# Optimization experiments

Hardware: AMD Instinct MI355X
Metric: run time of the kernel (lower is better)

Reference implementation:

```python
import jax, jax.numpy as jnp
import numpy as np

NUM_HEADS = 4
BN_EPS = 1e-5


def setup_inputs() -> dict:
    key = jax.random.key(0)
    k1, k2, k3 = jax.random.split(key, 3)
    B, C, H, W = 4, 512, 64, 64
    c_attn = 256
    x = jax.random.normal(k1, (B, C, H, W), dtype=jnp.float32)
    # 1x1 convs are plain channel matmuls: weight[out, in]
    w_qkv = jax.random.normal(k2, (3 * c_attn, c_attn), dtype=jnp.float32) * (c_attn ** -0.5)
    w_proj = jax.random.normal(k3, (c_attn, c_attn), dtype=jnp.float32) * (c_attn ** -0.5)
    gamma = jnp.ones((c_attn,), dtype=jnp.float32)
    beta = jnp.zeros((c_attn,), dtype=jnp.float32)
    return {"x": x, "w_qkv": w_qkv, "w_proj": w_proj, "gamma": gamma, "beta": beta}


def reference(x, w_qkv, w_proj, gamma, beta):
    B, C, H, W = x.shape
    c_attn = w_proj.shape[0]
    head_dim = c_attn // NUM_HEADS
    scale = head_dim ** -0.5
    N = H * W

    x_attn = x[:, :c_attn].reshape(B, c_attn, N)   # [B, c_attn, N]
    x_skip = x[:, c_attn:]                          # [B, c_skip, H, W]

    # 1x1 conv qkv (no bias): [B, 3*c_attn, N]
    qkv = jnp.einsum('oc,bcn->bon', w_qkv, x_attn)
    qkv = qkv.reshape(B, 3, NUM_HEADS, head_dim, N)
    q, k, v = qkv[:, 0], qkv[:, 1], qkv[:, 2]       # each [B, h, d, N]

    # attn[b,h,i,j] = sum_d q[b,h,d,i] * k[b,h,d,j] * scale
    attn = jnp.einsum('bhdn,bhdm->bhnm', q, k) * scale
    attn = jax.nn.softmax(attn, axis=-1)

    # out[b,h,d,i] = sum_j attn[b,h,i,j] * v[b,h,d,j]
    out = jnp.einsum('bhnm,bhdm->bhdn', attn, v).reshape(B, c_attn, N)

    # 1x1 conv proj (no bias)
    out = jnp.einsum('oc,bcn->bon', w_proj, out)

    # BatchNorm2d (training mode: batch statistics over B and spatial dims)
    mean = out.mean(axis=(0, 2), keepdims=True)
    var = out.var(axis=(0, 2), keepdims=True)  # biased variance, as torch BN
    out = (out - mean) * jax.lax.rsqrt(var + BN_EPS)
    out = out * gamma[None, :, None] + beta[None, :, None]

    out = out.reshape(B, c_attn, H, W)
    return jnp.concatenate([out, x_skip], axis=1)
```

## Files before the change

kernel.cpp:

```cpp
#include <hip/hip_runtime.h>
#include <stdint.h>

typedef float          f32x4  __attribute__((ext_vector_type(4)));
typedef __bf16         bf16x8 __attribute__((ext_vector_type(8)));
typedef unsigned short u16x4  __attribute__((ext_vector_type(4)));
typedef unsigned short u16x8  __attribute__((ext_vector_type(8)));

__device__ __forceinline__ float bf2f(unsigned short u) {
    union { uint32_t i; float f; } v; v.i = ((uint32_t)u) << 16; return v.f;
}
__device__ __forceinline__ unsigned short bfc(float f) {
    return __builtin_bit_cast(unsigned short, (__bf16)f);
}
__device__ __forceinline__ f32x4 mfma16(bf16x8 a, bf16x8 b, f32x4 c) {
    return __builtin_amdgcn_mfma_f32_16x16x32_bf16(a, b, c, 0, 0, 0);
}
__device__ __forceinline__ void async16(const unsigned short* g, unsigned short* l) {
    __builtin_amdgcn_global_load_lds(
        (const __attribute__((address_space(1))) void*)g,
        (__attribute__((address_space(3))) void*)l, 16, 0, 0);
}

#define QSC 0.18033688f

__global__ __launch_bounds__(256) void qkv_gemm(
    const float* __restrict__ x, const float* __restrict__ wqkv,
    unsigned short* __restrict__ Qb, unsigned short* __restrict__ Kb,
    unsigned short* __restrict__ Vb) {
    const int mt = blockIdx.x;
    const int nt = blockIdx.y;
    const int b  = blockIdx.z;
    const int o0 = mt * 128, n0 = nt * 128;
    __shared__ __align__(16) unsigned short Wt[128 * 72];
    __shared__ __align__(16) unsigned short Xt[128 * 72];
    const int t = threadIdx.x;
    const int lane = t & 63, w = t >> 6;
    const int wr = w >> 1, wc = w & 1;
    const int l15 = lane & 15, g = lane >> 4;

    f32x4 acc[4][4];
    const f32x4 zero = {0.f, 0.f, 0.f, 0.f};
    for (int i = 0; i < 4; i++) for (int j = 0; j < 4; j++) acc[i][j] = zero;

    for (int k0 = 0; k0 < 256; k0 += 64) {
        {
            const int row = t >> 3, col = (t & 7) * 8;
            #pragma unroll
            for (int r = 0; r < 4; r++) {
                const float* p = wqkv + (size_t)(o0 + row + r * 32) * 256 + k0 + col;
                f32x4 v0 = *(const f32x4*)p;
                f32x4 v1 = *(const f32x4*)(p + 4);
                u16x8 o8 = { bfc(v0[0]), bfc(v0[1]), bfc(v0[2]), bfc(v0[3]),
                             bfc(v1[0]), bfc(v1[1]), bfc(v1[2]), bfc(v1[3]) };
                *(u16x8*)(&Wt[(row + r * 32) * 72 + col]) = o8;
            }
        }
        {
            const int cl = t >> 4, nl = (t & 15) * 8;
            #pragma unroll
            for (int r = 0; r < 4; r++) {
                const int c = k0 + cl + r * 16;
                const float* p = x + (size_t)(b * 512 + c) * 4096 + n0 + nl;
                f32x4 v0 = *(const f32x4*)p;
                f32x4 v1 = *(const f32x4*)(p + 4);
                #pragma unroll
                for (int j = 0; j < 4; j++) Xt[(nl + j) * 72 + cl + r * 16] = bfc(v0[j]);
                #pragma unroll
                for (int j = 0; j < 4; j++) Xt[(nl + 4 + j) * 72 + cl + r * 16] = bfc(v1[j]);
            }
        }
        __syncthreads();
        #pragma unroll
        for (int kk = 0; kk < 2; kk++) {
            bf16x8 af[4], bfr[4];
            #pragma unroll
            for (int i = 0; i < 4; i++)
                af[i] = *(const bf16x8*)(&Wt[(wr * 64 + i * 16 + l15) * 72 + kk * 32 + g * 8]);
            #pragma unroll
            for (int j = 0; j < 4; j++)
                bfr[j] = *(const bf16x8*)(&Xt[(wc * 64 + j * 16 + l15) * 72 + kk * 32 + g * 8]);
            #pragma unroll
            for (int i = 0; i < 4; i++)
                #pragma unroll
                for (int j = 0; j < 4; j++)
                    acc[i][j] = mfma16(af[i], bfr[j], acc[i][j]);
        }
        __syncthreads();
    }

    #pragma unroll
    for (int i = 0; i < 4; i++) {
        const int o = o0 + wr * 64 + i * 16 + g * 4;
        #pragma unroll
        for (int j = 0; j < 4; j++) {
            const int n = n0 + wc * 64 + j * 16 + l15;
            f32x4 a = acc[i][j];
            if (o < 256) {
                u16x4 pv = { bfc(a[0] * QSC), bfc(a[1] * QSC), bfc(a[2] * QSC), bfc(a[3] * QSC) };
                const int h = o >> 6, d = o & 63;
                *(u16x4*)(&Qb[(((size_t)(b * 4 + h)) * 4096 + n) * 64 + d]) = pv;
            } else if (o < 512) {
                u16x4 pv = { bfc(a[0]), bfc(a[1]), bfc(a[2]), bfc(a[3]) };
                const int oo = o - 256; const int h = oo >> 6, d = oo & 63;
                *(u16x4*)(&Kb[(((size_t)(b * 4 + h)) * 4096 + n) * 64 + d]) = pv;
            } else {
                const int oo = o - 512; const int h = oo >> 6, d = oo & 63;
                const size_t base = (((size_t)(b * 4 + h)) * 64 + d) * 4096 + n;
                Vb[base] = bfc(a[0]); Vb[base + 4096] = bfc(a[1]);
                Vb[base + 8192] = bfc(a[2]); Vb[base + 12288] = bfc(a[3]);
            }
        }
    }
}

__global__ __launch_bounds__(256, 2) void flash_attn(
    const unsigned short* __restrict__ Qb, const unsigned short* __restrict__ Kb,
    const unsigned short* __restrict__ Vb, unsigned short* __restrict__ Opart,
    float* __restrict__ ml) {
    __shared__ __align__(16) unsigned short Kt[2][64 * 64];
    __shared__ __align__(16) unsigned short Vt[2][64 * 64];

    const int flat = (blockIdx.z * 16 + blockIdx.y) * 16 + blockIdx.x;
    const int nf = (flat & 7) * 64 + (flat >> 3);
    const int z  = nf >> 8;
    const int bh = (nf >> 4) & 15;
    const int nb = nf & 15;

    const int t = threadIdx.x, lane = t & 63, w = t >> 6;
    const int l15 = lane & 15, g = lane >> 4;
    const int xo = (l15 & 7) << 3;
    const int c0 = (g * 8) ^ xo, c1 = c0 ^ 32;
    const int vq = ((((g >> 1) ^ (l15 & 7)) << 3) | ((g & 1) << 2));

    const int rb = lane >> 3;
    const int cbe = ((lane & 7) ^ rb) << 3;
    const unsigned short* kgp = Kb + ((size_t)bh * 4096 + z * 2048 + w * 8 + rb) * 64 + cbe;
    const unsigned short* vgp = Vb + ((size_t)(bh * 64 + w * 8 + rb)) * 4096 + z * 2048 + cbe;

    auto stage = [&](int buf) {
        async16(kgp,          &Kt[buf][w * 512]);
        async16(kgp + 2048,   &Kt[buf][w * 512 + 2048]);
        async16(vgp,          &Vt[buf][w * 512]);
        async16(vgp + 131072, &Vt[buf][w * 512 + 2048]);
        kgp += 4096; vgp += 64;
    };

    bf16x8 qf[4][2];
    #pragma unroll
    for (int ntl = 0; ntl < 4; ++ntl) {
        const int nq = nb * 256 + w * 64 + ntl * 16 + l15;
        const unsigned short* qp = Qb + ((size_t)bh * 4096 + nq) * 64;
        qf[ntl][0] = *(const bf16x8*)(qp + g * 8);
        qf[ntl][1] = *(const bf16x8*)(qp + 32 + g * 8);
    }

    const bf16x8 ones8 = __builtin_bit_cast(bf16x8,
        (u16x8){0x3F80, 0x3F80, 0x3F80, 0x3F80, 0x3F80, 0x3F80, 0x3F80, 0x3F80});

    f32x4 of[4][4];
    f32x4 lf[4];
    const f32x4 zero = {0.f, 0.f, 0.f, 0.f};
    #pragma unroll
    for (int dt = 0; dt < 4; ++dt)
        #pragma unroll
        for (int ntl = 0; ntl < 4; ++ntl) of[dt][ntl] = zero;
    lf[0] = zero; lf[1] = zero; lf[2] = zero; lf[3] = zero;

    stage(0);
    __syncthreads();

    for (int itp = 0; itp < 16; ++itp) {
        #pragma unroll
        for (int cur = 0; cur < 2; ++cur) {
            if (itp * 2 + cur < 31) stage(cur ^ 1);

            bf16x8 ka[4][2], va[4][2];
            #pragma unroll
            for (int mt = 0; mt < 4; ++mt) {
                const int kro = (mt * 16 + l15) * 64;
                ka[mt][0] = *(const bf16x8*)(&Kt[cur][kro + c0]);
                ka[mt][1] = *(const bf16x8*)(&Kt[cur][kro + c1]);
            }
            #pragma unroll
            for (int dt = 0; dt < 4; ++dt) {
                const unsigned short* vr = &Vt[cur][l15 * 64 + dt * 1024];
                u16x4 w00 = *(const u16x4*)(vr + (vq ^ 0));
                u16x4 w01 = *(const u16x4*)(vr + (vq ^ 16));
                u16x4 w10 = *(const u16x4*)(vr + (vq ^ 32));
                u16x4 w11 = *(const u16x4*)(vr + (vq ^ 48));
                va[dt][0] = __builtin_bit_cast(bf16x8,
                    __builtin_shufflevector(w00, w01, 0, 1, 2, 3, 4, 5, 6, 7));
                va[dt][1] = __builtin_bit_cast(bf16x8,
                    __builtin_shufflevector(w10, w11, 0, 1, 2, 3, 4, 5, 6, 7));
            }

            #pragma unroll
            for (int ntl = 0; ntl < 4; ++ntl) {
                f32x4 st[4];
                __builtin_amdgcn_s_setprio(1);
                #pragma unroll
                for (int mt = 0; mt < 4; ++mt)
                    st[mt] = mfma16(ka[mt][1], qf[ntl][1],
                                    mfma16(ka[mt][0], qf[ntl][0], zero));
                __builtin_amdgcn_s_setprio(0);

                u16x4 q0 = { bfc(__builtin_amdgcn_exp2f(st[0][0])),
                             bfc(__builtin_amdgcn_exp2f(st[0][1])),
                             bfc(__builtin_amdgcn_exp2f(st[0][2])),
                             bfc(__builtin_amdgcn_exp2f(st[0][3])) };
                u16x4 q1 = { bfc(__builtin_amdgcn_exp2f(st[1][0])),
                             bfc(__builtin_amdgcn_exp2f(st[1][1])),
                             bfc(__builtin_amdgcn_exp2f(st[1][2])),
                             bfc(__builtin_amdgcn_exp2f(st[1][3])) };
                u16x4 q2 = { bfc(__builtin_amdgcn_exp2f(st[2][0])),
                             bfc(__builtin_amdgcn_exp2f(st[2][1])),
                             bfc(__builtin_amdgcn_exp2f(st[2][2])),
                             bfc(__builtin_amdgcn_exp2f(st[2][3])) };
                u16x4 q3 = { bfc(__builtin_amdgcn_exp2f(st[3][0])),
                             bfc(__builtin_amdgcn_exp2f(st[3][1])),
                             bfc(__builtin_amdgcn_exp2f(st[3][2])),
                             bfc(__builtin_amdgcn_exp2f(st[3][3])) };
                bf16x8 pb0 = __builtin_bit_cast(bf16x8,
                    __builtin_shufflevector(q0, q1, 0, 1, 2, 3, 4, 5, 6, 7));
                bf16x8 pb1 = __builtin_bit_cast(bf16x8,
                    __builtin_shufflevector(q2, q3, 0, 1, 2, 3, 4, 5, 6, 7));

                __builtin_amdgcn_s_setprio(1);
                lf[ntl] = mfma16(ones8, pb1, mfma16(ones8, pb0, lf[ntl]));
                #pragma unroll
                for (int dt = 0; dt < 4; ++dt)
                    of[dt][ntl] = mfma16(va[dt][1], pb1,
                                         mfma16(va[dt][0], pb0, of[dt][ntl]));
                __builtin_amdgcn_s_setprio(0);
            }
            __syncthreads();
        }
    }

    #pragma unroll
    for (int ntl = 0; ntl < 4; ++ntl) {
        const int nq = nb * 256 + w * 64 + ntl * 16 + l15;
        const size_t obase = ((size_t)((z * 16 + bh) * 4096 + nq)) * 64;
        #pragma unroll
        for (int dt = 0; dt < 4; ++dt) {
            u16x4 pv = { bfc(of[dt][ntl][0]), bfc(of[dt][ntl][1]),
                         bfc(of[dt][ntl][2]), bfc(of[dt][ntl][3]) };
            *(u16x4*)(&Opart[obase + dt * 16 + g * 4]) = pv;
        }
        if (g == 0) ml[z * 65536 + bh * 4096 + nq] = lf[ntl][0];
    }
}

__global__ __launch_bounds__(256) void proj_gemm(
    const unsigned short* __restrict__ Opart, const float* __restrict__ ml,
    const float* __restrict__ wproj,
    unsigned short* __restrict__ projbf, float* __restrict__ psum) {
    const int mt = blockIdx.x;
    const int nt = blockIdx.y;
    const int b  = blockIdx.z;
    const int o0 = mt * 128, n0 = nt * 128;
    __shared__ __align__(16) unsigned short Wt[128 * 72];
    __shared__ __align__(16) unsigned short Bt[128 * 72];
    const int t = threadIdx.x;
    const int lane = t & 63, w = t >> 6;
    const int wr = w >> 1, wc = w & 1;
    const int l15 = lane & 15, g = lane >> 4;

    f32x4 acc[4][4];
    const f32x4 zero = {0.f, 0.f, 0.f, 0.f};
    for (int i = 0; i < 4; i++) for (int j = 0; j < 4; j++) acc[i][j] = zero;

    for (int k0 = 0; k0 < 256; k0 += 64) {
        const int row = t >> 3, col = (t & 7) * 8;
        const int h = k0 >> 6;
        #pragma unroll
        for (int r = 0; r < 4; r++) {
            const float* p = wproj + (size_t)(o0 + row + r * 32) * 256 + k0 + col;
            f32x4 v0 = *(const f32x4*)p;
            f32x4 v1 = *(const f32x4*)(p + 4);
            u16x8 o8 = { bfc(v0[0]), bfc(v0[1]), bfc(v0[2]), bfc(v0[3]),
                         bfc(v1[0]), bfc(v1[1]), bfc(v1[2]), bfc(v1[3]) };
            *(u16x8*)(&Wt[(row + r * 32) * 72 + col]) = o8;
            const int n = n0 + row + r * 32;
            const int qidx = (b * 4 + h) * 4096 + n;
            const float inv = 1.f / (ml[qidx] + ml[65536 + qidx]);
            u16x8 m1 = *(const u16x8*)(Opart + (size_t)qidx * 64 + col);
            u16x8 m2 = *(const u16x8*)(Opart + 4194304u + (size_t)qidx * 64 + col);
            u16x8 a;
            #pragma unroll
            for (int j = 0; j < 8; ++j) a[j] = bfc((bf2f(m1[j]) + bf2f(m2[j])) * inv);
            *(u16x8*)(&Bt[(row + r * 32) * 72 + col]) = a;
        }
        __syncthreads();
        #pragma unroll
        for (int kk = 0; kk < 2; kk++) {
            bf16x8 af[4], bfr[4];
            #pragma unroll
            for (int i = 0; i < 4; i++)
                af[i] = *(const bf16x8*)(&Wt[(wr * 64 + i * 16 + l15) * 72 + kk * 32 + g * 8]);
            #pragma unroll
            for (int j = 0; j < 4; j++)
                bfr[j] = *(const bf16x8*)(&Bt[(wc * 64 + j * 16 + l15) * 72 + kk * 32 + g * 8]);
            #pragma unroll
            for (int i = 0; i < 4; i++)
                #pragma unroll
                for (int j = 0; j < 4; j++)
                    acc[i][j] = mfma16(af[i], bfr[j], acc[i][j]);
        }
        __syncthreads();
    }

    #pragma unroll
    for (int i = 0; i < 4; i++) {
        const int o = o0 + wr * 64 + i * 16 + g * 4;
        #pragma unroll
        for (int j = 0; j < 4; j++) {
            const int n = n0 + wc * 64 + j * 16 + l15;
            f32x4 a = acc[i][j];
            #pragma unroll
            for (int r = 0; r < 4; r++)
                projbf[((size_t)(b * 256 + o + r)) * 4096 + n] = bfc(a[r]);
        }
        f32x4 s = acc[i][0], q;
        #pragma unroll
        for (int r = 0; r < 4; ++r) q[r] = acc[i][0][r] * acc[i][0][r];
        #pragma unroll
        for (int j = 1; j < 4; ++j)
            #pragma unroll
            for (int r = 0; r < 4; ++r) {
                s[r] += acc[i][j][r];
                q[r] = fmaf(acc[i][j][r], acc[i][j][r], q[r]);
            }
        #pragma unroll
        for (int m = 1; m < 16; m <<= 1) {
            #pragma unroll
            for (int r = 0; r < 4; ++r) {
                s[r] += __shfl_xor(s[r], m, 64);
                q[r] += __shfl_xor(q[r], m, 64);
            }
        }
        if (l15 == 0) {
            const int slot = (b * 32 + nt) * 2 + wc;
            *(f32x4*)(&psum[slot * 256 + o]) = s;
            *(f32x4*)(&psum[65536 + slot * 256 + o]) = q;
        }
    }
}

__global__ __launch_bounds__(256) void bn_finalize(const float* __restrict__ psum,
                                                   float* __restrict__ stats) {
    const int o = blockIdx.x, t = threadIdx.x;
    const int lane = t & 63, w = t >> 6;
    float s = psum[t * 256 + o];
    float q = psum[65536 + t * 256 + o];
    #pragma unroll
    for (int m = 1; m < 64; m <<= 1) {
        s += __shfl_xor(s, m, 64);
        q += __shfl_xor(q, m, 64);
    }
    __shared__ float red[8];
    if (lane == 0) { red[w] = s; red[4 + w] = q; }
    __syncthreads();
    if (t == 0) {
        const float S = red[0] + red[1] + red[2] + red[3];
        const float Q = red[4] + red[5] + red[6] + red[7];
        const float mean = S * (1.f / 16384.f);
        const float var = Q * (1.f / 16384.f) - mean * mean;
        stats[o] = mean;
        stats[256 + o] = rsqrtf(var + 1e-5f);
    }
}

__global__ __launch_bounds__(256) void bn_apply(
    const unsigned short* __restrict__ projbf, const float* __restrict__ stats,
    const float* __restrict__ gamma, const float* __restrict__ beta,
    const float* __restrict__ x, float* __restrict__ out) {
    const size_t idx8 = ((size_t)blockIdx.x * 256 + threadIdx.x) * 8;
    const int n  = (int)(idx8 & 4095);
    const int ch = (int)((idx8 >> 12) & 511);
    const int b  = (int)(idx8 >> 21);
    if (ch < 256) {
        const float mean = stats[ch], rstd = stats[256 + ch];
        const float sc = gamma[ch] * rstd;
        const float sh = beta[ch] - mean * sc;
        u16x8 pv = *(const u16x8*)(projbf + (((size_t)(b * 256 + ch)) << 12) + n);
        f32x4 o0, o1;
        #pragma unroll
        for (int j = 0; j < 4; j++) { o0[j] = bf2f(pv[j]) * sc + sh; o1[j] = bf2f(pv[4 + j]) * sc + sh; }
        *(f32x4*)(out + idx8) = o0;
        *(f32x4*)(out + idx8 + 4) = o1;
    } else {
        *(f32x4*)(out + idx8)     = *(const f32x4*)(x + idx8);
        *(f32x4*)(out + idx8 + 4) = *(const f32x4*)(x + idx8 + 4);
    }
}

extern "C" void kernel_launch(void* const* d_in, const int* in_sizes, int n_in,
                              void* d_out, int out_size, void* d_ws, size_t ws_size,
                              hipStream_t stream) {
    const float* x     = (const float*)d_in[0];
    const float* wqkv  = (const float*)d_in[1];
    const float* wproj = (const float*)d_in[2];
    const float* gamma = (const float*)d_in[3];
    const float* beta  = (const float*)d_in[4];
    float* out = (float*)d_out;

    char* ws = (char*)d_ws;
    unsigned short* Qb     = (unsigned short*)(ws);
    unsigned short* Kb     = (unsigned short*)(ws + (8ull  << 20));
    unsigned short* Vb     = (unsigned short*)(ws + (16ull << 20));
    unsigned short* Opart  = (unsigned short*)(ws + (24ull << 20));
    float*          ml     = (float*)(ws + (41ull << 20));
    unsigned short* projbf = (unsigned short*)(ws);
    float*          psum   = (float*)(ws + (9ull << 20));
    float*          stats  = (float*)(ws + (9ull << 20) + (768u << 10));

    qkv_gemm   <<<dim3(6, 32, 4),  256, 0, stream>>>(x, wqkv, Qb, Kb, Vb);
    flash_attn <<<dim3(16, 16, 2), 256, 0, stream>>>(Qb, Kb, Vb, Opart, ml);
    proj_gemm  <<<dim3(2, 32, 4),  256, 0, stream>>>(Opart, ml, wproj, projbf, psum);
    bn_finalize<<<256,             256, 0, stream>>>(psum, stats);
    bn_apply   <<<4096,            256, 0, stream>>>(projbf, stats, gamma, beta, x, out);
}
```

Measured before the change: 136.1 us.

## Split attention KV range four ways and stash partial outputs in output buffer

The flash attention kernel now splits the key/value sequence into four chunks instead of two, launching twice as many blocks, each processing half as many tiles. Occupancy hint is raised to four blocks per CU. Partial outputs for the upper two splits are written into the final output buffer as scratch so workspace stays bounded, and the projection kernel sums four partials and four denominators. This trades more partial-output traffic and reduction work for better CU utilization and shorter per-block latency.

```diff
diff --git a/kernel.cpp b/kernel.cpp
--- a/kernel.cpp
+++ b/kernel.cpp
@@ -113,15 +113,15 @@
     }
 }
 
-__global__ __launch_bounds__(256, 2) void flash_attn(
+__global__ __launch_bounds__(256, 4) void flash_attn(
     const unsigned short* __restrict__ Qb, const unsigned short* __restrict__ Kb,
-    const unsigned short* __restrict__ Vb, unsigned short* __restrict__ Opart,
-    float* __restrict__ ml) {
+    const unsigned short* __restrict__ Vb, unsigned short* __restrict__ Olo,
+    unsigned short* __restrict__ Ohi, float* __restrict__ ml) {
     __shared__ __align__(16) unsigned short Kt[2][64 * 64];
     __shared__ __align__(16) unsigned short Vt[2][64 * 64];
 
     const int flat = (blockIdx.z * 16 + blockIdx.y) * 16 + blockIdx.x;
-    const int nf = (flat & 7) * 64 + (flat >> 3);
+    const int nf = (flat & 7) * 128 + (flat >> 3);
     const int z  = nf >> 8;
     const int bh = (nf >> 4) & 15;
     const int nb = nf & 15;
@@ -134,8 +134,8 @@
 
     const int rb = lane >> 3;
     const int cbe = ((lane & 7) ^ rb) << 3;
-    const unsigned short* kgp = Kb + ((size_t)bh * 4096 + z * 2048 + w * 8 + rb) * 64 + cbe;
-    const unsigned short* vgp = Vb + ((size_t)(bh * 64 + w * 8 + rb)) * 4096 + z * 2048 + cbe;
+    const unsigned short* kgp = Kb + ((size_t)bh * 4096 + z * 1024 + w * 8 + rb) * 64 + cbe;
+    const unsigned short* vgp = Vb + ((size_t)(bh * 64 + w * 8 + rb)) * 4096 + z * 1024 + cbe;
 
     auto stage = [&](int buf) {
         async16(kgp,          &Kt[buf][w * 512]);
@@ -169,10 +169,10 @@
     stage(0);
     __syncthreads();
 
-    for (int itp = 0; itp < 16; ++itp) {
+    for (int itp = 0; itp < 8; ++itp) {
         #pragma unroll
         for (int cur = 0; cur < 2; ++cur) {
-            if (itp * 2 + cur < 31) stage(cur ^ 1);
+            if (itp * 2 + cur < 15) stage(cur ^ 1);
 
             bf16x8 ka[4][2], va[4][2];
             #pragma unroll
@@ -237,23 +237,24 @@
         }
     }
 
+    unsigned short* Obase = (z & 2) ? Ohi : Olo;
     #pragma unroll
     for (int ntl = 0; ntl < 4; ++ntl) {
         const int nq = nb * 256 + w * 64 + ntl * 16 + l15;
-        const size_t obase = ((size_t)((z * 16 + bh) * 4096 + nq)) * 64;
+        const size_t obase = ((size_t)(((z & 1) * 16 + bh) * 4096 + nq)) * 64;
         #pragma unroll
         for (int dt = 0; dt < 4; ++dt) {
             u16x4 pv = { bfc(of[dt][ntl][0]), bfc(of[dt][ntl][1]),
                          bfc(of[dt][ntl][2]), bfc(of[dt][ntl][3]) };
-            *(u16x4*)(&Opart[obase + dt * 16 + g * 4]) = pv;
+            *(u16x4*)(&Obase[obase + dt * 16 + g * 4]) = pv;
         }
         if (g == 0) ml[z * 65536 + bh * 4096 + nq] = lf[ntl][0];
     }
 }
 
 __global__ __launch_bounds__(256) void proj_gemm(
-    const unsigned short* __restrict__ Opart, const float* __restrict__ ml,
-    const float* __restrict__ wproj,
+    const unsigned short* __restrict__ Olo, const unsigned short* __restrict__ Ohi,
+    const float* __restrict__ ml, const float* __restrict__ wproj,
     unsigned short* __restrict__ projbf, float* __restrict__ psum) {
     const int mt = blockIdx.x;
     const int nt = blockIdx.y;
@@ -283,12 +284,16 @@
             *(u16x8*)(&Wt[(row + r * 32) * 72 + col]) = o8;
             const int n = n0 + row + r * 32;
             const int qidx = (b * 4 + h) * 4096 + n;
-            const float inv = 1.f / (ml[qidx] + ml[65536 + qidx]);
-            u16x8 m1 = *(const u16x8*)(Opart + (size_t)qidx * 64 + col);
-            u16x8 m2 = *(const u16x8*)(Opart + 4194304u + (size_t)qidx * 64 + col);
+            const float inv = 1.f / (ml[qidx] + ml[65536 + qidx] +
+                                     ml[131072 + qidx] + ml[196608 + qidx]);
+            u16x8 m0 = *(const u16x8*)(Olo + (size_t)qidx * 64 + col);
+            u16x8 m1 = *(const u16x8*)(Olo + 4194304u + (size_t)qidx * 64 + col);
+            u16x8 m2 = *(const u16x8*)(Ohi + (size_t)qidx * 64 + col);
+            u16x8 m3 = *(const u16x8*)(Ohi + 4194304u + (size_t)qidx * 64 + col);
             u16x8 a;
             #pragma unroll
-            for (int j = 0; j < 8; ++j) a[j] = bfc((bf2f(m1[j]) + bf2f(m2[j])) * inv);
+            for (int j = 0; j < 8; ++j)
+                a[j] = bfc((bf2f(m0[j]) + bf2f(m1[j]) + bf2f(m2[j]) + bf2f(m3[j])) * inv);
             *(u16x8*)(&Bt[(row + r * 32) * 72 + col]) = a;
         }
         __syncthreads();
@@ -409,15 +414,16 @@
     unsigned short* Qb     = (unsigned short*)(ws);
     unsigned short* Kb     = (unsigned short*)(ws + (8ull  << 20));
     unsigned short* Vb     = (unsigned short*)(ws + (16ull << 20));
-    unsigned short* Opart  = (unsigned short*)(ws + (24ull << 20));
-    float*          ml     = (float*)(ws + (41ull << 20));
+    unsigned short* Olo    = (unsigned short*)(ws + (24ull << 20));
+    float*          ml     = (float*)(ws + (40ull << 20));
+    unsigned short* Ohi    = (unsigned short*)d_out;
     unsigned short* projbf = (unsigned short*)(ws);
-    float*          psum   = (float*)(ws + (9ull << 20));
-    float*          stats  = (float*)(ws + (9ull << 20) + (768u << 10));
+    float*          psum   = (float*)(ws + (8ull << 20));
+    float*          stats  = (float*)(ws + (9ull << 20));
 
     qkv_gemm   <<<dim3(6, 32, 4),  256, 0, stream>>>(x, wqkv, Qb, Kb, Vb);
-    flash_attn <<<dim3(16, 16, 2), 256, 0, stream>>>(Qb, Kb, Vb, Opart, ml);
-    proj_gemm  <<<dim3(2, 32, 4),  256, 0, stream>>>(Opart, ml, wproj, projbf, psum);
+    flash_attn <<<dim3(16, 16, 4), 256, 0, stream>>>(Qb, Kb, Vb, Olo, Ohi, ml);
+    proj_gemm  <<<dim3(2, 32, 4),  256, 0, stream>>>(Olo, Ohi, ml, wproj, projbf, psum);
     bn_finalize<<<256,             256, 0, stream>>>(psum, stats);
     bn_apply   <<<4096,            256, 0, stream>>>(projbf, stats, gamma, beta, x, out);
 }
```

Result: slower. 531.5 us (+290.6%).
